# Optimization experiments

Measured on AMD Instinct MI355X. Metric: run time of the kernel, lower is better.

The kernel has to match this reference:

```python
import jax, jax.numpy as jnp
import numpy as np

B, LINES, NREG, D, L, K, CATS = 256, 64, 64, 1024, 64, 16, 2
EPS = 1e-5

_idx = np.arange(K)
# modular digit-wise add / sub mixing tables: M[i,j,m] = 1 iff (i op j) mod K == m
M_ADD = jnp.asarray(((_idx[:, None] + _idx[None, :]) % K)[..., None] == _idx[None, None, :], dtype=jnp.float32)
M_SUB = jnp.asarray(((_idx[:, None] - _idx[None, :]) % K)[..., None] == _idx[None, None, :], dtype=jnp.float32)


def _ln(x, g, b):
    m = x.mean(-1, keepdims=True)
    v = ((x - m) ** 2).mean(-1, keepdims=True)
    return (x - m) / jnp.sqrt(v + EPS) * g + b


def setup_inputs() -> dict:
    key = jax.random.key(0)
    ks = jax.random.split(key, 12)
    p = jax.random.uniform(ks[0], (B, LINES, CATS))
    opcode_probs = p / p.sum(-1, keepdims=True)
    registers = jax.random.normal(ks[1], (B, NREG, D))
    k_write = jax.random.normal(ks[2], (B, LINES, D))
    q_read = jax.random.normal(ks[3], (B, LINES, 2, D))
    cond_distribution = jax.random.uniform(ks[4], (B, LINES, 4))
    gate = jax.random.uniform(ks[5], (B, LINES, 1))
    s = 0.02
    F = L * K
    return {
        'opcode_probs': opcode_probs, 'registers': registers, 'k_write': k_write,
        'q_read': q_read, 'cond_distribution': cond_distribution, 'gate': gate,
        'ln1_g': jnp.ones((D,)), 'ln1_b': jnp.zeros((D,)),
        'w1': jax.random.normal(ks[6], (D, F)) * s, 'b1': jnp.zeros((F,)),
        'ln2_g': jnp.ones((D,)), 'ln2_b': jnp.zeros((D,)),
        'w2': jax.random.normal(ks[7], (D, F)) * s, 'b2': jnp.zeros((F,)),
        'w_res': jax.random.normal(ks[8], (F, D)) * s, 'b_res': jnp.zeros((D,)),
        'lno_g': jnp.ones((D,)), 'lno_b': jnp.zeros((D,)),
    }


def reference(opcode_probs, registers, k_write, q_read, cond_distribution, gate,
              ln1_g, ln1_b, w1, b1, ln2_g, ln2_b, w2, b2, w_res, b_res, lno_g, lno_b):
    scale = 1.0 / jnp.sqrt(jnp.asarray(D, jnp.float32))

    def digit_op(x, y, M):
        # x,y: (b,l,k) digit distributions -> (b,l,k) modular arithmetic result
        return jnp.einsum('bli,blj,ijm->blm', x, y, M)

    def step(R, xs):
        prob, q, kw, g = xs  # (b,2) (b,2,d) (b,d) (b,1)
        # attention read of two operands from register memory
        attn = jax.nn.softmax(jnp.einsum('bqd,brd->bqr', q, R) * scale, axis=-1)
        op_s = jnp.einsum('bqr,brd->bqd', attn, R)
        x = jax.nn.softmax((_ln(op_s[:, 0], ln1_g, ln1_b) @ w1 + b1).reshape(-1, L, K), axis=-1)
        y = jax.nn.softmax((_ln(op_s[:, 1], ln2_g, ln2_b) @ w2 + b2).reshape(-1, L, K), axis=-1)
        outs = jnp.stack([digit_op(x, y, M_ADD), digit_op(x, y, M_SUB)], axis=1)  # (b,2,l,k)
        mix = jnp.einsum('bn,bnlk->blk', prob, outs).reshape(-1, L * K)
        value = _ln(mix @ w_res + b_res, lno_g, lno_b)  # (b,d)
        # attention write-back with gate
        w = jax.nn.softmax(jnp.einsum('bd,brd->br', kw, R) * scale, axis=-1)
        gw = (g * w)[..., None]  # (b,r,1)
        R = R * (1.0 - gw) + gw * value[:, None, :]
        return R, None

    xs = (jnp.moveaxis(opcode_probs, 1, 0), jnp.moveaxis(q_read, 1, 0),
          jnp.moveaxis(k_write, 1, 0), jnp.moveaxis(gate, 1, 0))
    R, _ = jax.lax.scan(step, registers, xs)
    return R
```

## Files before the change

### kernel.cpp

```cpp
#include <hip/hip_runtime.h>
#include <hip/hip_bf16.h>

#define BB 256
#define LINES 64
#define NREG 64
#define DD 1024
#define FF 1024

constexpr float EPS = 1e-5f;
constexpr float SCALE = 0.03125f;

typedef __bf16 bf16_t;
typedef bf16_t bf16x8 __attribute__((ext_vector_type(8)));
typedef unsigned short us16x8 __attribute__((ext_vector_type(8)));
typedef float f32x4 __attribute__((ext_vector_type(4)));
typedef unsigned u32x4v __attribute__((ext_vector_type(4)));
typedef unsigned long long u64;

#define WS_W1T   0u
#define WS_W2T   (2u << 20)
#define WS_WRT   (4u << 20)
#define WS_XNP   (6u << 20)
#define WS_MIXP  (7u << 20)
#define WS_GT    ((7u << 20) + (1u << 19))
#define WS_CTR   ((8u << 20) + (1u << 19))
#define WS_NEED  (WS_CTR + 1024u)

#define SM_WV    0
#define SM_AT0P  256
#define SM_AT1P  512
#define SM_SC0   768
#define SM_SC1   1024
#define SM_SCW   1280
#define SM_RED   1536
#define SM_DYN   2048
#define SM_OSB   SM_DYN
#define SM_AT0   SM_DYN
#define SM_AT1   (SM_DYN + 32768)
#define SM_RED2  (SM_DYN + 65536)
#define SM_PRE   (SM_DYN + 65536 + 13056)
#define SM_VAL   (SM_DYN + 65536 + 13056 + 8448)
#define SM_SIZE  (SM_VAL + 4352)

__device__ __forceinline__ float wred(float v) {
#pragma unroll
  for (int m = 32; m >= 1; m >>= 1) v += __shfl_xor(v, m);
  return v;
}
__device__ __forceinline__ float wmax64(float v) {
#pragma unroll
  for (int m = 32; m >= 1; m >>= 1) v = fmaxf(v, __shfl_xor(v, m));
  return v;
}

__device__ __forceinline__ void st_llc32(void* p, unsigned v) {
  asm volatile("global_store_dword %0, %1, off sc0 sc1" :: "v"(p), "v"(v) : "memory");
}
__device__ __forceinline__ void st_llc16b(void* p, unsigned short v) {
  unsigned vv = v;
  asm volatile("global_store_short %0, %1, off sc0 sc1" :: "v"(p), "v"(vv) : "memory");
}
__device__ __forceinline__ unsigned ld_llc32(const void* p) {
  unsigned r;
  asm volatile("global_load_dword %0, %1, off sc0 sc1\n\ts_waitcnt vmcnt(0)"
               : "=v"(r) : "v"(p) : "memory");
  return r;
}
__device__ __forceinline__ void ld_llc_4x8(const void* p, u64& a, u64& b, u64& c, u64& d) {
  asm volatile(
      "global_load_dwordx2 %0, %4, off sc0 sc1\n\t"
      "global_load_dwordx2 %1, %4, off offset:8 sc0 sc1\n\t"
      "global_load_dwordx2 %2, %4, off offset:16 sc0 sc1\n\t"
      "global_load_dwordx2 %3, %4, off offset:24 sc0 sc1\n\t"
      "s_waitcnt vmcnt(0)"
      : "=&v"(a), "=&v"(b), "=&v"(c), "=&v"(d) : "v"(p) : "memory");
}
__device__ __forceinline__ u32x4v ld_llc_16(const void* p) {
  u32x4v r;
  asm volatile("global_load_dwordx4 %0, %1, off sc0 sc1\n\ts_waitcnt vmcnt(0)"
               : "=v"(r) : "v"(p) : "memory");
  return r;
}

__device__ __forceinline__ void group_barrier(unsigned* ctr, int tid, unsigned target) {
  asm volatile("s_waitcnt vmcnt(0)" ::: "memory");
  __syncthreads();
  if (tid == 0) {
    __hip_atomic_fetch_add(ctr, 1u, __ATOMIC_RELAXED, __HIP_MEMORY_SCOPE_AGENT);
    while (ld_llc32(ctr) < target) __builtin_amdgcn_s_sleep(2);
  }
  __syncthreads();
}

__global__ __launch_bounds__(256) void transcvt(const float* __restrict__ w1,
                                                const float* __restrict__ w2,
                                                const float* __restrict__ wr,
                                                bf16_t* __restrict__ out) {
  __shared__ float tl[64][65];
  const float* src = (blockIdx.z == 0) ? w1 : (blockIdx.z == 1) ? w2 : wr;
  bf16_t* dst = out + (size_t)blockIdx.z * (1u << 20);
  const int i0 = blockIdx.x * 64, j0 = blockIdx.y * 64;
  const int t = threadIdx.x;
#pragma unroll
  for (int it = 0; it < 4; ++it) {
    int r = (t >> 4) + it * 16;
    int c4 = (t & 15) * 4;
    const float4 v = *reinterpret_cast<const float4*>(&src[(size_t)(i0 + r) * 1024 + j0 + c4]);
    tl[r][c4] = v.x; tl[r][c4 + 1] = v.y; tl[r][c4 + 2] = v.z; tl[r][c4 + 3] = v.w;
  }
  __syncthreads();
  const int orow = t >> 2, seg = t & 3;
  bf16x8 v0, v1;
#pragma unroll
  for (int u = 0; u < 8; ++u) {
    v0[u] = (bf16_t)tl[seg * 16 + u][orow];
    v1[u] = (bf16_t)tl[seg * 16 + 8 + u][orow];
  }
  bf16_t* dp = dst + (size_t)(j0 + orow) * 1024 + i0 + seg * 16;
  *reinterpret_cast<bf16x8*>(dp) = v0;
  *reinterpret_cast<bf16x8*>(dp + 8) = v1;
}

__global__ __launch_bounds__(1024, 4) void interp3(
    const float* __restrict__ opcode_probs, const float* __restrict__ Rin,
    const float* __restrict__ k_write, const float* __restrict__ q_read,
    const float* __restrict__ gate,
    const float* __restrict__ ln1_g, const float* __restrict__ ln1_b, const float* __restrict__ b1,
    const float* __restrict__ ln2_g, const float* __restrict__ ln2_b, const float* __restrict__ b2,
    const float* __restrict__ b_res, const float* __restrict__ lno_g, const float* __restrict__ lno_b,
    char* __restrict__ ws, float* __restrict__ Rout) {
  __shared__ __align__(16) char smem[SM_SIZE];
  float* wvp  = (float*)(smem + SM_WV);
  float* at0p = (float*)(smem + SM_AT0P);
  float* at1p = (float*)(smem + SM_AT1P);
  float* sc0p = (float*)(smem + SM_SC0);
  float* sc1p = (float*)(smem + SM_SC1);
  float* scwp = (float*)(smem + SM_SCW);
  float* redp = (float*)(smem + SM_RED);

  const int b = blockIdx.x;
  const int g = b >> 4, m = b & 15;
  const int bq = b;
  const int tid = threadIdx.x;
  const int w = tid >> 6, lane = tid & 63;
  const int ln15 = lane & 15, kgrp = lane >> 4;

  const bf16_t* w1t = (const bf16_t*)(ws + WS_W1T);
  const bf16_t* w2t = (const bf16_t*)(ws + WS_W2T);
  const bf16_t* wrt = (const bf16_t*)(ws + WS_WRT);
  unsigned* xnp   = (unsigned*)(ws + WS_XNP);
  bf16_t*  mixp   = (bf16_t*)(ws + WS_MIXP);
  unsigned* gtw   = (unsigned*)(ws + WS_GT);
  unsigned* ctr   = (unsigned*)(ws + WS_CTR) + g * 16;

  float Rr_[4][16];
  {
    const float* Rsrc = Rin + (size_t)bq * (NREG * DD);
#pragma unroll
    for (int rr = 0; rr < 4; ++rr) {
#pragma unroll
      for (int c = 0; c < 4; ++c) {
        float4 v = *(const float4*)(Rsrc + (size_t)(4 * w + rr) * DD + lane * 16 + c * 4);
        Rr_[rr][c * 4 + 0] = v.x; Rr_[rr][c * 4 + 1] = v.y;
        Rr_[rr][c * 4 + 2] = v.z; Rr_[rr][c * 4 + 3] = v.w;
      }
    }
  }

  unsigned nbar = 0;

  for (int t = 0; t < LINES; ++t) {
    {
      const float* qb = q_read + ((size_t)bq * LINES + t) * (2 * DD);
      const float* kb = k_write + ((size_t)bq * LINES + t) * DD;
      const int dbase = lane * 16;
#pragma unroll
      for (int v = 0; v < 3; ++v) {
        const float* src = (v == 0) ? qb : (v == 1) ? (qb + DD) : kb;
        float* dst = (v == 0) ? sc0p : (v == 1) ? sc1p : scwp;
        float qv[16];
#pragma unroll
        for (int c = 0; c < 4; ++c) {
          float4 t4 = *(const float4*)(src + dbase + c * 4);
          qv[c * 4 + 0] = t4.x; qv[c * 4 + 1] = t4.y;
          qv[c * 4 + 2] = t4.z; qv[c * 4 + 3] = t4.w;
        }
#pragma unroll
        for (int rr = 0; rr < 4; ++rr) {
          float s = 0.f;
#pragma unroll
          for (int j = 0; j < 16; ++j) s = fmaf(Rr_[rr][j], qv[j], s);
          s = wred(s);
          if (lane == 0) dst[4 * w + rr] = s * SCALE;
        }
      }
    }
    __syncthreads();
    if (w < 3) {
      const float* src = (w == 0) ? sc0p : (w == 1) ? sc1p : scwp;
      float* dst = (w == 0) ? at0p : (w == 1) ? at1p : wvp;
      float v = src[lane];
      float mx = wmax64(v);
      float e = expf(v - mx);
      float s = wred(e);
      dst[lane] = e / s;
    }
    __syncthreads();
    float os0, os1;
    {
      float p0[16], p1[16];
#pragma unroll
      for (int j = 0; j < 16; ++j) { p0[j] = 0.f; p1[j] = 0.f; }
#pragma unroll
      for (int rr = 0; rr < 4; ++rr) {
        float a0 = at0p[4 * w + rr], a1 = at1p[4 * w + rr];
#pragma unroll
        for (int j = 0; j < 16; ++j) {
          p0[j] = fmaf(a0, Rr_[rr][j], p0[j]);
          p1[j] = fmaf(a1, Rr_[rr][j], p1[j]);
        }
      }
      float* osb = (float*)(smem + SM_OSB);
      const int rp = (tid >> 4) * 17 + (tid & 15);
#pragma unroll
      for (int j = 0; j < 16; ++j) osb[w * 1088 + lane * 17 + j] = p0[j];
      __syncthreads();
      os0 = 0.f;
#pragma unroll
      for (int ww = 0; ww < 16; ++ww) os0 += osb[ww * 1088 + rp];
      __syncthreads();
#pragma unroll
      for (int j = 0; j < 16; ++j) osb[w * 1088 + lane * 17 + j] = p1[j];
      __syncthreads();
      os1 = 0.f;
#pragma unroll
      for (int ww = 0; ww < 16; ++ww) os1 += osb[ww * 1088 + rp];
    }
    {
      float s0 = wred(os0), qq0 = wred(os0 * os0);
      float s1 = wred(os1), qq1 = wred(os1 * os1);
      if (lane == 0) { redp[w*4] = s0; redp[w*4+1] = qq0; redp[w*4+2] = s1; redp[w*4+3] = qq1; }
      __syncthreads();
      float S0 = 0, Q0 = 0, S1 = 0, Q1 = 0;
#pragma unroll
      for (int i = 0; i < 16; ++i) { S0 += redp[i*4]; Q0 += redp[i*4+1]; S1 += redp[i*4+2]; Q1 += redp[i*4+3]; }
      float m0 = S0 * (1.f / DD), v0 = fmaxf(Q0 * (1.f / DD) - m0 * m0, 0.f);
      float m1 = S1 * (1.f / DD), v1 = fmaxf(Q1 * (1.f / DD) - m1 * m1, 0.f);
      float xn0v = (os0 - m0) * rsqrtf(v0 + EPS) * ln1_g[tid] + ln1_b[tid];
      float xn1v = (os1 - m1) * rsqrtf(v1 + EPS) * ln2_g[tid] + ln2_b[tid];
      unsigned pw = (unsigned)__builtin_bit_cast(unsigned short, (bf16_t)xn0v)
                  | ((unsigned)__builtin_bit_cast(unsigned short, (bf16_t)xn1v) << 16);
      st_llc32(&xnp[((size_t)g * 16 + m) * DD + tid], pw);
    }
    group_barrier(ctr, tid, 16u * (++nbar));

    {
      const char* base = (const char*)(xnp + (size_t)g * (16 * DD));
#pragma unroll
      for (int c = 0; c < 2; ++c) {
        int ch = tid + c * 1024;
        int row = ch >> 7, k16 = ch & 127;
        u64 w0, w1v, w2v, w3v;
        ld_llc_4x8(base + (size_t)row * 4096 + k16 * 32, w0, w1v, w2v, w3v);
        us16x8 v0, v1;
        v0[0] = (unsigned short)w0;          v1[0] = (unsigned short)(w0 >> 16);
        v0[1] = (unsigned short)(w0 >> 32);  v1[1] = (unsigned short)(w0 >> 48);
        v0[2] = (unsigned short)w1v;         v1[2] = (unsigned short)(w1v >> 16);
        v0[3] = (unsigned short)(w1v >> 32); v1[3] = (unsigned short)(w1v >> 48);
        v0[4] = (unsigned short)w2v;         v1[4] = (unsigned short)(w2v >> 16);
        v0[5] = (unsigned short)(w2v >> 32); v1[5] = (unsigned short)(w2v >> 48);
        v0[6] = (unsigned short)w3v;         v1[6] = (unsigned short)(w3v >> 16);
        v0[7] = (unsigned short)(w3v >> 32); v1[7] = (unsigned short)(w3v >> 48);
        unsigned byte = (unsigned)(row * 2048 + k16 * 16) ^ ((unsigned)(row & 7) << 4);
        *(us16x8*)(smem + SM_AT0 + byte) = v0;
        *(us16x8*)(smem + SM_AT1 + byte) = v1;
      }
    }
    __syncthreads();

#pragma unroll
    for (int gm = 0; gm < 2; ++gm) {
      const char* atile = smem + (gm ? SM_AT1 : SM_AT0);
      const int ns = w & 3, ks = w >> 2;
      const bf16_t* bsrc = (gm ? w2t : w1t) + (size_t)(64 * m + ns * 16 + ln15) * DD;
      f32x4 acc = {0.f, 0.f, 0.f, 0.f};
#pragma unroll
      for (int kc = 0; kc < 8; ++kc) {
        int kb = ks * 256 + kc * 32 + kgrp * 8;
        unsigned abyte = ((unsigned)(ln15 * 2048 + kb * 2)) ^ ((unsigned)(ln15 & 7) << 4);
        bf16x8 av = *(const bf16x8*)(atile + abyte);
        bf16x8 bv = *(const bf16x8*)(bsrc + kb);
        acc = __builtin_amdgcn_mfma_f32_16x16x32_bf16(av, bv, acc, 0, 0, 0);
      }
      __syncthreads();
      float* red2 = (float*)(smem + SM_RED2);
      if (ks > 0) {
#pragma unroll
        for (int r2 = 0; r2 < 4; ++r2)
          red2[((ks - 1) * 4 + ns) * (16 * 17) + (kgrp * 4 + r2) * 17 + ln15] = acc[r2];
      }
      __syncthreads();
      if (ks == 0) {
        float* prep = (float*)(smem + SM_PRE) + gm * (16 * 66);
#pragma unroll
        for (int r2 = 0; r2 < 4; ++r2) {
          int crow = kgrp * 4 + r2;
          float v = acc[r2];
#pragma unroll
          for (int kk = 0; kk < 3; ++kk)
            v += red2[(kk * 4 + ns) * (16 * 17) + crow * 17 + ln15];
          prep[crow * 66 + ns * 16 + ln15] = v;
        }
      }
      __syncthreads();
    }
    {
      float* prep = (float*)(smem + SM_PRE);
      const int bb2 = w, c = lane;
      float xp = prep[bb2 * 66 + c] + b1[64 * m + c];
      float yp = prep[16 * 66 + bb2 * 66 + c] + b2[64 * m + c];
      float mx1 = xp, mx2 = yp;
#pragma unroll
      for (int msk = 1; msk < 16; msk <<= 1) {
        mx1 = fmaxf(mx1, __shfl_xor(mx1, msk));
        mx2 = fmaxf(mx2, __shfl_xor(mx2, msk));
      }
      float e1 = expf(xp - mx1), e2 = expf(yp - mx2);
      float s1 = e1, s2 = e2;
#pragma unroll
      for (int msk = 1; msk < 16; msk <<= 1) {
        s1 += __shfl_xor(s1, msk);
        s2 += __shfl_xor(s2, msk);
      }
      float x = e1 / s1, y = e2 / s2;
      int mm = lane & 15, basel = lane & ~15;
      float addv = 0.f, subv = 0.f;
#pragma unroll
      for (int i = 0; i < 16; ++i) {
        float xi = __shfl(x, basel + i);
        float ya = __shfl(y, basel + ((mm - i) & 15));
        float ys = __shfl(y, basel + ((i - mm) & 15));
        addv = fmaf(xi, ya, addv);
        subv = fmaf(xi, ys, subv);
      }
      int q2 = g * 16 + bb2;
      const float* pr = opcode_probs + ((size_t)q2 * LINES + t) * 2;
      float mix = pr[0] * addv + pr[1] * subv;
      st_llc16b(&mixp[((size_t)g * 16 + bb2) * DD + 64 * m + c],
                __builtin_bit_cast(unsigned short, (bf16_t)mix));
    }
    group_barrier(ctr, tid, 16u * (++nbar));

    {
      const char* base = (const char*)(mixp + (size_t)g * (16 * DD));
#pragma unroll
      for (int c = 0; c < 2; ++c) {
        int ch = tid + c * 1024;
        int row = ch >> 7, k16 = ch & 127;
        u32x4v v = ld_llc_16(base + (size_t)row * 2048 + k16 * 16);
        unsigned byte = (unsigned)(row * 2048 + k16 * 16) ^ ((unsigned)(row & 7) << 4);
        *(u32x4v*)(smem + SM_AT0 + byte) = v;
      }
      __syncthreads();
      const int ns = w & 3, ks = w >> 2;
      const bf16_t* bsrc = wrt + (size_t)(64 * m + ns * 16 + ln15) * DD;
      f32x4 acc = {0.f, 0.f, 0.f, 0.f};
#pragma unroll
      for (int kc = 0; kc < 8; ++kc) {
        int kb = ks * 256 + kc * 32 + kgrp * 8;
        unsigned abyte = ((unsigned)(ln15 * 2048 + kb * 2)) ^ ((unsigned)(ln15 & 7) << 4);
        bf16x8 av = *(const bf16x8*)(smem + SM_AT0 + abyte);
        bf16x8 bv = *(const bf16x8*)(bsrc + kb);
        acc = __builtin_amdgcn_mfma_f32_16x16x32_bf16(av, bv, acc, 0, 0, 0);
      }
      __syncthreads();
      float* red2 = (float*)(smem + SM_RED2);
      if (ks > 0) {
#pragma unroll
        for (int r2 = 0; r2 < 4; ++r2)
          red2[((ks - 1) * 4 + ns) * (16 * 17) + (kgrp * 4 + r2) * 17 + ln15] = acc[r2];
      }
      __syncthreads();
      if (ks == 0) {
        int f = 64 * m + ns * 16 + ln15;
#pragma unroll
        for (int r2 = 0; r2 < 4; ++r2) {
          int crow = kgrp * 4 + r2;
          float v = acc[r2];
#pragma unroll
          for (int kk = 0; kk < 3; ++kk)
            v += red2[(kk * 4 + ns) * (16 * 17) + crow * 17 + ln15];
          st_llc32(&gtw[((size_t)g * 16 + crow) * DD + f],
                   __builtin_bit_cast(unsigned, v + b_res[f]));
        }
      }
    }
    group_barrier(ctr, tid, 16u * (++nbar));

    {
      float xv = __builtin_bit_cast(float, ld_llc32(&gtw[((size_t)g * 16 + m) * DD + tid]));
      float s1 = wred(xv), s2 = wred(xv * xv);
      if (lane == 0) { redp[w * 2] = s1; redp[w * 2 + 1] = s2; }
      __syncthreads();
      float S = 0.f, Q = 0.f;
#pragma unroll
      for (int i = 0; i < 16; ++i) { S += redp[i * 2]; Q += redp[i * 2 + 1]; }
      float mn = S * (1.f / DD), vr = fmaxf(Q * (1.f / DD) - mn * mn, 0.f);
      float vv = (xv - mn) * rsqrtf(vr + EPS) * lno_g[tid] + lno_b[tid];
      float* valp = (float*)(smem + SM_VAL);
      valp[(tid >> 4) * 17 + (tid & 15)] = vv;
    }
    __syncthreads();
    {
      float gtv = gate[(size_t)bq * LINES + t];
      const float* valp = (const float*)(smem + SM_VAL);
      float vvj[16];
#pragma unroll
      for (int j = 0; j < 16; ++j) vvj[j] = valp[lane * 17 + j];
#pragma unroll
      for (int rr = 0; rr < 4; ++rr) {
        float gg = gtv * wvp[4 * w + rr];
#pragma unroll
        for (int j = 0; j < 16; ++j)
          Rr_[rr][j] = Rr_[rr][j] * (1.f - gg) + gg * vvj[j];
      }
    }
  }

  {
    float* Rdst = Rout + (size_t)bq * (NREG * DD);
#pragma unroll
    for (int rr = 0; rr < 4; ++rr) {
#pragma unroll
      for (int c = 0; c < 4; ++c) {
        float4 v;
        v.x = Rr_[rr][c * 4 + 0]; v.y = Rr_[rr][c * 4 + 1];
        v.z = Rr_[rr][c * 4 + 2]; v.w = Rr_[rr][c * 4 + 3];
        *(float4*)(Rdst + (size_t)(4 * w + rr) * DD + lane * 16 + c * 4) = v;
      }
    }
  }
}

__global__ __launch_bounds__(1024) void interp_fb(
    const float* __restrict__ opcode_probs, const float* __restrict__ k_write,
    const float* __restrict__ q_read, const float* __restrict__ gate,
    const float* __restrict__ ln1_g, const float* __restrict__ ln1_b,
    const float* __restrict__ w1, const float* __restrict__ b1,
    const float* __restrict__ ln2_g, const float* __restrict__ ln2_b,
    const float* __restrict__ w2, const float* __restrict__ b2,
    const float* __restrict__ w_res, const float* __restrict__ b_res,
    const float* __restrict__ lno_g, const float* __restrict__ lno_b,
    float* __restrict__ R) {
  __shared__ float q0s[DD], q1s[DD], kws[DD];
  __shared__ float sc0[NREG], sc1[NREG], scw[NREG];
  __shared__ float at0[NREG], at1[NREG], wv[NREG];
  __shared__ float xn0[DD], xn1[DD];
  __shared__ float mixs[FF];
  __shared__ float val[DD];
  __shared__ float red[64];
  const int b = blockIdx.x;
  const int tid = threadIdx.x;
  const int w = tid >> 6, lane = tid & 63;
  float* Rb = R + (size_t)b * NREG * DD;
  for (int t = 0; t < LINES; ++t) {
    const float* qb = q_read + ((size_t)b * LINES + t) * 2 * DD;
    const float* kb = k_write + ((size_t)b * LINES + t) * DD;
    q0s[tid] = qb[tid]; q1s[tid] = qb[DD + tid]; kws[tid] = kb[tid];
    __syncthreads();
#pragma unroll
    for (int rr = 0; rr < 4; ++rr) {
      int r = w * 4 + rr;
      const float* Rr = Rb + (size_t)r * DD;
      float a0 = 0.f, a1 = 0.f, aw = 0.f;
#pragma unroll
      for (int j = 0; j < 16; ++j) {
        int d = j * 64 + lane;
        float rv = Rr[d];
        a0 += rv * q0s[d]; a1 += rv * q1s[d]; aw += rv * kws[d];
      }
      a0 = wred(a0); a1 = wred(a1); aw = wred(aw);
      if (lane == 0) { sc0[r] = a0 * SCALE; sc1[r] = a1 * SCALE; scw[r] = aw * SCALE; }
    }
    __syncthreads();
    if (w < 3) {
      const float* src = (w == 0) ? sc0 : (w == 1) ? sc1 : scw;
      float* dst = (w == 0) ? at0 : (w == 1) ? at1 : wv;
      float v = src[lane];
      float mx = wmax64(v);
      float e = expf(v - mx);
      float s = wred(e);
      dst[lane] = e / s;
    }
    __syncthreads();
    float os0 = 0.f, os1 = 0.f;
#pragma unroll 4
    for (int r = 0; r < NREG; ++r) {
      float rv = Rb[(size_t)r * DD + tid];
      os0 += at0[r] * rv; os1 += at1[r] * rv;
    }
    {
      float s0 = wred(os0), qq0 = wred(os0 * os0);
      float s1 = wred(os1), qq1 = wred(os1 * os1);
      if (lane == 0) { red[w*4] = s0; red[w*4+1] = qq0; red[w*4+2] = s1; red[w*4+3] = qq1; }
      __syncthreads();
      float S0 = 0, Q0 = 0, S1 = 0, Q1 = 0;
#pragma unroll
      for (int i = 0; i < 16; ++i) { S0 += red[i*4]; Q0 += red[i*4+1]; S1 += red[i*4+2]; Q1 += red[i*4+3]; }
      float m0 = S0 / DD, v0 = fmaxf(Q0 / DD - m0 * m0, 0.f);
      float m1 = S1 / DD, v1 = fmaxf(Q1 / DD - m1 * m1, 0.f);
      xn0[tid] = (os0 - m0) * rsqrtf(v0 + EPS) * ln1_g[tid] + ln1_b[tid];
      xn1[tid] = (os1 - m1) * rsqrtf(v1 + EPS) * ln2_g[tid] + ln2_b[tid];
      __syncthreads();
    }
    float p1v = b1[tid], p2v = b2[tid];
    {
      const float* c1 = w1 + tid;
      const float* c2 = w2 + tid;
#pragma unroll 4
      for (int d = 0; d < DD; ++d) {
        p1v += xn0[d] * c1[(size_t)d * FF];
        p2v += xn1[d] * c2[(size_t)d * FF];
      }
    }
    {
      int mmm = lane & 15, basel = lane & ~15;
      float mx1 = p1v, mx2 = p2v;
      for (int msk = 1; msk < 16; msk <<= 1) {
        mx1 = fmaxf(mx1, __shfl_xor(mx1, msk));
        mx2 = fmaxf(mx2, __shfl_xor(mx2, msk));
      }
      float e1 = expf(p1v - mx1), e2 = expf(p2v - mx2);
      float s1 = e1, s2 = e2;
      for (int msk = 1; msk < 16; msk <<= 1) { s1 += __shfl_xor(s1, msk); s2 += __shfl_xor(s2, msk); }
      float x = e1 / s1, y = e2 / s2;
      float addv = 0.f, subv = 0.f;
#pragma unroll
      for (int i = 0; i < 16; ++i) {
        float xi = __shfl(x, basel + i);
        float ya = __shfl(y, basel + ((mmm - i) & 15));
        float ys = __shfl(y, basel + ((i - mmm) & 15));
        addv += xi * ya; subv += xi * ys;
      }
      const float* pr = opcode_probs + ((size_t)b * LINES + t) * 2;
      mixs[tid] = pr[0] * addv + pr[1] * subv;
    }
    __syncthreads();
    float acc = b_res[tid];
    {
      const float* cr = w_res + tid;
#pragma unroll 4
      for (int f = 0; f < FF; ++f) acc += mixs[f] * cr[(size_t)f * DD];
    }
    {
      float s1 = wred(acc), s2 = wred(acc * acc);
      if (lane == 0) { red[w*2] = s1; red[w*2+1] = s2; }
      __syncthreads();
      float S = 0, Q = 0;
#pragma unroll
      for (int i = 0; i < 16; ++i) { S += red[i*2]; Q += red[i*2+1]; }
      float mn = S / DD, vr = fmaxf(Q / DD - mn * mn, 0.f);
      val[tid] = (acc - mn) * rsqrtf(vr + EPS) * lno_g[tid] + lno_b[tid];
      __syncthreads();
    }
    {
      float gt_ = gate[(size_t)b * LINES + t];
      float vv = val[tid];
#pragma unroll 4
      for (int r = 0; r < NREG; ++r) {
        float gg = gt_ * wv[r];
        size_t idx = (size_t)r * DD + tid;
        Rb[idx] = Rb[idx] * (1.f - gg) + gg * vv;
      }
    }
    __syncthreads();
  }
}

extern "C" void kernel_launch(void* const* d_in, const int* in_sizes, int n_in,
                              void* d_out, int out_size, void* d_ws, size_t ws_size,
                              hipStream_t stream) {
  const float* opcode = (const float*)d_in[0];
  const float* registers = (const float*)d_in[1];
  const float* k_write = (const float*)d_in[2];
  const float* q_read = (const float*)d_in[3];
  const float* gate = (const float*)d_in[5];
  const float* ln1_g = (const float*)d_in[6];
  const float* ln1_b = (const float*)d_in[7];
  const float* w1 = (const float*)d_in[8];
  const float* b1 = (const float*)d_in[9];
  const float* ln2_g = (const float*)d_in[10];
  const float* ln2_b = (const float*)d_in[11];
  const float* w2 = (const float*)d_in[12];
  const float* b2 = (const float*)d_in[13];
  const float* w_res = (const float*)d_in[14];
  const float* b_res = (const float*)d_in[15];
  const float* lno_g = (const float*)d_in[16];
  const float* lno_b = (const float*)d_in[17];
  float* R = (float*)d_out;

  if (ws_size >= (size_t)WS_NEED) {
    transcvt<<<dim3(16, 16, 3), 256, 0, stream>>>(w1, w2, w_res, (bf16_t*)d_ws);
    hipMemsetAsync((char*)d_ws + WS_CTR, 0, 1024, stream);
    interp3<<<BB, 1024, 0, stream>>>(opcode, registers, k_write, q_read, gate,
                                     ln1_g, ln1_b, b1, ln2_g, ln2_b, b2,
                                     b_res, lno_g, lno_b, (char*)d_ws, R);
  } else {
    hipMemcpyAsync(R, registers, (size_t)BB * NREG * DD * sizeof(float),
                   hipMemcpyDeviceToDevice, stream);
    interp_fb<<<BB, 1024, 0, stream>>>(opcode, k_write, q_read, gate, ln1_g, ln1_b,
                                       w1, b1, ln2_g, ln2_b, w2, b2, w_res, b_res,
                                       lno_g, lno_b, R);
  }
}
```

Measured before the change: 4.138 ms.

## Prefetch next-step q/k into LDS, batch LLC loads, remap block-to-slice

New measurement: 3.953 ms. -4.5%, faster.

```diff
diff --git a/kernel.cpp b/kernel.cpp
--- a/kernel.cpp
+++ b/kernel.cpp
@@ -40,7 +40,8 @@
 #define SM_RED2  (SM_DYN + 65536)
 #define SM_PRE   (SM_DYN + 65536 + 13056)
 #define SM_VAL   (SM_DYN + 65536 + 13056 + 8448)
-#define SM_SIZE  (SM_VAL + 4352)
+#define SM_QPF   (SM_VAL + 4352)
+#define SM_SIZE  (SM_QPF + 15360)
 
 __device__ __forceinline__ float wred(float v) {
 #pragma unroll
@@ -66,20 +67,21 @@
                : "=v"(r) : "v"(p) : "memory");
   return r;
 }
-__device__ __forceinline__ void ld_llc_4x8(const void* p, u64& a, u64& b, u64& c, u64& d) {
+__device__ __forceinline__ void ld_llc_4x8_nw(const void* p, u64& a, u64& b, u64& c, u64& d) {
   asm volatile(
       "global_load_dwordx2 %0, %4, off sc0 sc1\n\t"
       "global_load_dwordx2 %1, %4, off offset:8 sc0 sc1\n\t"
       "global_load_dwordx2 %2, %4, off offset:16 sc0 sc1\n\t"
-      "global_load_dwordx2 %3, %4, off offset:24 sc0 sc1\n\t"
-      "s_waitcnt vmcnt(0)"
+      "global_load_dwordx2 %3, %4, off offset:24 sc0 sc1"
       : "=&v"(a), "=&v"(b), "=&v"(c), "=&v"(d) : "v"(p) : "memory");
 }
-__device__ __forceinline__ u32x4v ld_llc_16(const void* p) {
-  u32x4v r;
-  asm volatile("global_load_dwordx4 %0, %1, off sc0 sc1\n\ts_waitcnt vmcnt(0)"
-               : "=v"(r) : "v"(p) : "memory");
-  return r;
+__device__ __forceinline__ void ld_llc_16_nw(const void* p, u32x4v& r) {
+  asm volatile("global_load_dwordx4 %0, %1, off sc0 sc1"
+               : "=&v"(r) : "v"(p) : "memory");
+}
+__device__ __forceinline__ void wait_vm0() {
+  asm volatile("s_waitcnt vmcnt(0)" ::: "memory");
+  __builtin_amdgcn_sched_barrier(0);
 }
 
 __device__ __forceinline__ void group_barrier(unsigned* ctr, int tid, unsigned target) {
@@ -139,7 +141,9 @@
   float* redp = (float*)(smem + SM_RED);
 
   const int b = blockIdx.x;
-  const int g = b >> 4, m = b & 15;
+  const int g = b >> 4;
+  const int j = b & 15;
+  const int m = ((b & 7) << 1) | ((b >> 3) & 1);
   const int bq = b;
   const int tid = threadIdx.x;
   const int w = tid >> 6, lane = tid & 63;
@@ -167,21 +171,30 @@
     }
   }
 
+  {
+    const float* qb = q_read + ((size_t)bq * LINES + 0) * (2 * DD);
+    const float* kb = k_write + ((size_t)bq * LINES + 0) * DD;
+    float* qpf = (float*)(smem + SM_QPF);
+    const int pidx = (tid >> 4) * 20 + (tid & 15);
+    qpf[pidx] = qb[tid];
+    qpf[1280 + pidx] = qb[DD + tid];
+    qpf[2560 + pidx] = kb[tid];
+  }
+  __syncthreads();
+
   unsigned nbar = 0;
 
   for (int t = 0; t < LINES; ++t) {
     {
-      const float* qb = q_read + ((size_t)bq * LINES + t) * (2 * DD);
-      const float* kb = k_write + ((size_t)bq * LINES + t) * DD;
-      const int dbase = lane * 16;
+      const float* qpf = (const float*)(smem + SM_QPF);
+      const int pb = lane * 20;
 #pragma unroll
       for (int v = 0; v < 3; ++v) {
-        const float* src = (v == 0) ? qb : (v == 1) ? (qb + DD) : kb;
         float* dst = (v == 0) ? sc0p : (v == 1) ? sc1p : scwp;
         float qv[16];
 #pragma unroll
         for (int c = 0; c < 4; ++c) {
-          float4 t4 = *(const float4*)(src + dbase + c * 4);
+          float4 t4 = *(const float4*)(qpf + v * 1280 + pb + c * 4);
           qv[c * 4 + 0] = t4.x; qv[c * 4 + 1] = t4.y;
           qv[c * 4 + 2] = t4.z; qv[c * 4 + 3] = t4.w;
         }
@@ -189,7 +202,7 @@
         for (int rr = 0; rr < 4; ++rr) {
           float s = 0.f;
 #pragma unroll
-          for (int j = 0; j < 16; ++j) s = fmaf(Rr_[rr][j], qv[j], s);
+          for (int jj = 0; jj < 16; ++jj) s = fmaf(Rr_[rr][jj], qv[jj], s);
           s = wred(s);
           if (lane == 0) dst[4 * w + rr] = s * SCALE;
         }
@@ -210,27 +223,27 @@
     {
       float p0[16], p1[16];
 #pragma unroll
-      for (int j = 0; j < 16; ++j) { p0[j] = 0.f; p1[j] = 0.f; }
+      for (int jj = 0; jj < 16; ++jj) { p0[jj] = 0.f; p1[jj] = 0.f; }
 #pragma unroll
       for (int rr = 0; rr < 4; ++rr) {
         float a0 = at0p[4 * w + rr], a1 = at1p[4 * w + rr];
 #pragma unroll
-        for (int j = 0; j < 16; ++j) {
-          p0[j] = fmaf(a0, Rr_[rr][j], p0[j]);
-          p1[j] = fmaf(a1, Rr_[rr][j], p1[j]);
+        for (int jj = 0; jj < 16; ++jj) {
+          p0[jj] = fmaf(a0, Rr_[rr][jj], p0[jj]);
+          p1[jj] = fmaf(a1, Rr_[rr][jj], p1[jj]);
         }
       }
       float* osb = (float*)(smem + SM_OSB);
       const int rp = (tid >> 4) * 17 + (tid & 15);
 #pragma unroll
-      for (int j = 0; j < 16; ++j) osb[w * 1088 + lane * 17 + j] = p0[j];
+      for (int jj = 0; jj < 16; ++jj) osb[w * 1088 + lane * 17 + jj] = p0[jj];
       __syncthreads();
       os0 = 0.f;
 #pragma unroll
       for (int ww = 0; ww < 16; ++ww) os0 += osb[ww * 1088 + rp];
       __syncthreads();
 #pragma unroll
-      for (int j = 0; j < 16; ++j) osb[w * 1088 + lane * 17 + j] = p1[j];
+      for (int jj = 0; jj < 16; ++jj) osb[w * 1088 + lane * 17 + jj] = p1[jj];
       __syncthreads();
       os1 = 0.f;
 #pragma unroll
@@ -250,31 +263,41 @@
       float xn1v = (os1 - m1) * rsqrtf(v1 + EPS) * ln2_g[tid] + ln2_b[tid];
       unsigned pw = (unsigned)__builtin_bit_cast(unsigned short, (bf16_t)xn0v)
                   | ((unsigned)__builtin_bit_cast(unsigned short, (bf16_t)xn1v) << 16);
-      st_llc32(&xnp[((size_t)g * 16 + m) * DD + tid], pw);
+      st_llc32(&xnp[((size_t)g * 16 + j) * DD + tid], pw);
     }
     group_barrier(ctr, tid, 16u * (++nbar));
 
     {
       const char* base = (const char*)(xnp + (size_t)g * (16 * DD));
-#pragma unroll
-      for (int c = 0; c < 2; ++c) {
-        int ch = tid + c * 1024;
-        int row = ch >> 7, k16 = ch & 127;
-        u64 w0, w1v, w2v, w3v;
-        ld_llc_4x8(base + (size_t)row * 4096 + k16 * 32, w0, w1v, w2v, w3v);
+      const int row = tid >> 7, k16 = tid & 127;
+      u64 a0, a1, a2, a3, c0, c1, c2, c3;
+      ld_llc_4x8_nw(base + (size_t)row * 4096 + k16 * 32, a0, a1, a2, a3);
+      ld_llc_4x8_nw(base + (size_t)(row + 8) * 4096 + k16 * 32, c0, c1, c2, c3);
+      wait_vm0();
+#pragma unroll
+      for (int h = 0; h < 2; ++h) {
+        u64 x0 = h ? c0 : a0, x1 = h ? c1 : a1, x2 = h ? c2 : a2, x3 = h ? c3 : a3;
+        int r = row + h * 8;
         us16x8 v0, v1;
-        v0[0] = (unsigned short)w0;          v1[0] = (unsigned short)(w0 >> 16);
-        v0[1] = (unsigned short)(w0 >> 32);  v1[1] = (unsigned short)(w0 >> 48);
-        v0[2] = (unsigned short)w1v;         v1[2] = (unsigned short)(w1v >> 16);
-        v0[3] = (unsigned short)(w1v >> 32); v1[3] = (unsigned short)(w1v >> 48);
-        v0[4] = (unsigned short)w2v;         v1[4] = (unsigned short)(w2v >> 16);
-        v0[5] = (unsigned short)(w2v >> 32); v1[5] = (unsigned short)(w2v >> 48);
-        v0[6] = (unsigned short)w3v;         v1[6] = (unsigned short)(w3v >> 16);
-        v0[7] = (unsigned short)(w3v >> 32); v1[7] = (unsigned short)(w3v >> 48);
-        unsigned byte = (unsigned)(row * 2048 + k16 * 16) ^ ((unsigned)(row & 7) << 4);
+        v0[0] = (unsigned short)x0;         v1[0] = (unsigned short)(x0 >> 16);
+        v0[1] = (unsigned short)(x0 >> 32); v1[1] = (unsigned short)(x0 >> 48);
+        v0[2] = (unsigned short)x1;         v1[2] = (unsigned short)(x1 >> 16);
+        v0[3] = (unsigned short)(x1 >> 32); v1[3] = (unsigned short)(x1 >> 48);
+        v0[4] = (unsigned short)x2;         v1[4] = (unsigned short)(x2 >> 16);
+        v0[5] = (unsigned short)(x2 >> 32); v1[5] = (unsigned short)(x2 >> 48);
+        v0[6] = (unsigned short)x3;         v1[6] = (unsigned short)(x3 >> 16);
+        v0[7] = (unsigned short)(x3 >> 32); v1[7] = (unsigned short)(x3 >> 48);
+        unsigned byte = (unsigned)(r * 2048 + k16 * 16) ^ ((unsigned)(r & 7) << 4);
         *(us16x8*)(smem + SM_AT0 + byte) = v0;
         *(us16x8*)(smem + SM_AT1 + byte) = v1;
       }
+    }
+    float pf0, pf1, pf2;
+    {
+      int tn = (t + 1 < LINES) ? (t + 1) : (LINES - 1);
+      const float* qb2 = q_read + ((size_t)bq * LINES + tn) * (2 * DD);
+      const float* kb2 = k_write + ((size_t)bq * LINES + tn) * DD;
+      pf0 = qb2[tid]; pf1 = qb2[DD + tid]; pf2 = kb2[tid];
     }
     __syncthreads();
 
@@ -353,14 +376,15 @@
 
     {
       const char* base = (const char*)(mixp + (size_t)g * (16 * DD));
-#pragma unroll
-      for (int c = 0; c < 2; ++c) {
-        int ch = tid + c * 1024;
-        int row = ch >> 7, k16 = ch & 127;
-        u32x4v v = ld_llc_16(base + (size_t)row * 2048 + k16 * 16);
-        unsigned byte = (unsigned)(row * 2048 + k16 * 16) ^ ((unsigned)(row & 7) << 4);
-        *(u32x4v*)(smem + SM_AT0 + byte) = v;
-      }
+      const int row = tid >> 7, k16 = tid & 127;
+      u32x4v va, vb;
+      ld_llc_16_nw(base + (size_t)row * 2048 + k16 * 16, va);
+      ld_llc_16_nw(base + (size_t)(row + 8) * 2048 + k16 * 16, vb);
+      wait_vm0();
+      unsigned byte0 = (unsigned)(row * 2048 + k16 * 16) ^ ((unsigned)(row & 7) << 4);
+      unsigned byte1 = (unsigned)((row + 8) * 2048 + k16 * 16) ^ ((unsigned)(row & 7) << 4);
+      *(u32x4v*)(smem + SM_AT0 + byte0) = va;
+      *(u32x4v*)(smem + SM_AT0 + byte1) = vb;
       __syncthreads();
       const int ns = w & 3, ks = w >> 2;
       const bf16_t* bsrc = wrt + (size_t)(64 * m + ns * 16 + ln15) * DD;
@@ -398,7 +422,7 @@
     group_barrier(ctr, tid, 16u * (++nbar));
 
     {
-      float xv = __builtin_bit_cast(float, ld_llc32(&gtw[((size_t)g * 16 + m) * DD + tid]));
+      float xv = __builtin_bit_cast(float, ld_llc32(&gtw[((size_t)g * 16 + j) * DD + tid]));
       float s1 = wred(xv), s2 = wred(xv * xv);
       if (lane == 0) { redp[w * 2] = s1; redp[w * 2 + 1] = s2; }
       __syncthreads();
@@ -416,15 +440,21 @@
       const float* valp = (const float*)(smem + SM_VAL);
       float vvj[16];
 #pragma unroll
-      for (int j = 0; j < 16; ++j) vvj[j] = valp[lane * 17 + j];
+      for (int jj = 0; jj < 16; ++jj) vvj[jj] = valp[lane * 17 + jj];
 #pragma unroll
       for (int rr = 0; rr < 4; ++rr) {
         float gg = gtv * wvp[4 * w + rr];
 #pragma unroll
-        for (int j = 0; j < 16; ++j)
-          Rr_[rr][j] = Rr_[rr][j] * (1.f - gg) + gg * vvj[j];
-      }
-    }
+        for (int jj = 0; jj < 16; ++jj)
+          Rr_[rr][jj] = Rr_[rr][jj] * (1.f - gg) + gg * vvj[jj];
+      }
+      float* qpf = (float*)(smem + SM_QPF);
+      const int pidx = (tid >> 4) * 20 + (tid & 15);
+      qpf[pidx] = pf0;
+      qpf[1280 + pidx] = pf1;
+      qpf[2560 + pidx] = pf2;
+    }
+    __syncthreads();
   }
 
   {
@@ -474,8 +504,8 @@
       const float* Rr = Rb + (size_t)r * DD;
       float a0 = 0.f, a1 = 0.f, aw = 0.f;
 #pragma unroll
-      for (int j = 0; j < 16; ++j) {
-        int d = j * 64 + lane;
+      for (int jj = 0; jj < 16; ++jj) {
+        int d = jj * 64 + lane;
         float rv = Rr[d];
         a0 += rv * q0s[d]; a1 += rv * q1s[d]; aw += rv * kws[d];
       }
```
